# Kernel optimization log

Measured on AMD Instinct MI355X. Metric: run time of the kernel, lower is better.

Reference implementation:

```python
import jax, jax.numpy as jnp
import numpy as np
from jax import lax

EPS = 1e-06
K = 7  # kernel_size
C1 = 0.01 ** 2
C2 = 0.03 ** 2

_SOBEL_X = jnp.array([[-1.0, 0.0, 1.0], [-2.0, 0.0, 2.0], [-1.0, 0.0, 1.0]], dtype=jnp.float32).reshape(1, 1, 3, 3)
_SOBEL_Y = jnp.array([[-1.0, -2.0, -1.0], [0.0, 0.0, 0.0], [1.0, 2.0, 1.0]], dtype=jnp.float32).reshape(1, 1, 3, 3)


def _conv3x3(x, w):
    # NCHW cross-correlation with zero padding=1 (matches F.conv2d)
    return lax.conv_general_dilated(
        x, w, window_strides=(1, 1), padding=[(1, 1), (1, 1)],
        dimension_numbers=('NCHW', 'OIHW', 'NCHW'))


def _box(x):
    # avg_pool2d(k, stride=1, pad=k//2, count_include_pad=True):
    # sum over zero-padded window, divide by k*k everywhere.
    p = K // 2
    s = lax.reduce_window(x, jnp.float32(0.0), lax.add,
                          window_dimensions=(1, 1, K, K),
                          window_strides=(1, 1, 1, 1),
                          padding=[(0, 0), (0, 0), (p, p), (p, p)])
    return s / jnp.float32(K * K)


def _grad_mag(x):
    gx = _conv3x3(x, _SOBEL_X)
    gy = _conv3x3(x, _SOBEL_Y)
    return jnp.sqrt(gx * gx + gy * gy + EPS)


def setup_inputs() -> dict:
    key = jax.random.key(0)
    k1, k2 = jax.random.split(key)
    B, H, W = 64, 512, 512
    pred = jax.random.normal(k1, (B, 1, H, W), dtype=jnp.float32)
    target = jax.random.normal(k2, (B, 1, H, W), dtype=jnp.float32)
    min_target = jnp.zeros((B,), dtype=jnp.float32)
    max_target = jnp.ones((B,), dtype=jnp.float32)
    return {"pred": pred, "target": target, "min_target": min_target, "max_target": max_target}


def reference(pred, target, min_target, max_target):
    B = pred.shape[0]
    mn = min_target.reshape(B, 1, 1, 1)
    mx = max_target.reshape(B, 1, 1, 1)
    dr = jnp.maximum(mx - mn, EPS)
    p = (pred - mn) / dr
    t = (target - mn) / dr

    gp = _grad_mag(p)
    gt = _grad_mag(t)

    mu_p = _box(p)
    mu_t = _box(t)
    luminance = (2.0 * mu_p * mu_t + C1) / (mu_p * mu_p + mu_t * mu_t + C1)

    mu_gp = _box(gp)
    mu_gt = _box(gt)
    sig_p = _box(gp * gp) - mu_gp * mu_gp
    sig_t = _box(gt * gt) - mu_gt * mu_gt
    sig_x = _box(gp * gt) - mu_gp * mu_gt
    cs = (2.0 * sig_x + C2) / (sig_p + sig_t + C2)

    return 1.0 - jnp.mean(luminance * cs)
```

## Files before the change

kernel.cpp:

```cpp
#include <hip/hip_runtime.h>
#include <hip/hip_fp16.h>
#include <math.h>


constexpr int NT = 256;
constexpr float EPS_F = 1e-6f;
constexpr float C1S = 2401.0f * 0.0001f;
constexpr float C2S = 2401.0f * 0.0009f;

union U4 { uint4 u; __half2 h[4]; };
union F4U { float4 v; float a[4]; };

__device__ __forceinline__ __half2 h2swap(__half2 x) {
    unsigned u = __builtin_bit_cast(unsigned, x);
    u = (u >> 16) | (u << 16);
    return __builtin_bit_cast(__half2, u);
}

__device__ __forceinline__ float ssim_px(__half2 apt, __half2 ag, __half2 agg, __half2 agx) {
    float2 vpt = __half22float2(apt);
    float2 vg  = __half22float2(ag);
    float2 vgg = __half22float2(agg);
    float  vgx = __low2float(agx);
    float lum_n = 2.0f * vpt.x * vpt.y + C1S;
    float lum_d = vpt.x * vpt.x + vpt.y * vpt.y + C1S;
    float cs_n  = 2.0f * (49.0f * vgx - vg.x * vg.y) + C2S;
    float cs_d  = 49.0f * (vgg.x + vgg.y) - vg.x * vg.x - vg.y * vg.y + C2S;
    return lum_n * cs_n * __builtin_amdgcn_rcpf(lum_d * cs_d);
}

__global__ __launch_bounds__(NT, 4)
void gssim_strip(const float* __restrict__ pred, const float* __restrict__ target,
                 const float* __restrict__ mn_arr, const float* __restrict__ mx_arr,
                 float* __restrict__ partial) {
    constexpr int H = 512, W = 512;
    __shared__ alignas(16) __half2 spt[40][44];
    __shared__ alignas(16) __half2 hsAll[32][41][4];
    __shared__ float red[4];

    const int blk = blockIdx.x;
    const int b   = blk >> 4;
    const int gy0 = (blk & 15) * 32;
    const int tid = threadIdx.x;

    const float mn     = mn_arr[b];
    const float inv_dr = 1.0f / fmaxf(mx_arr[b] - mn, EPS_F);
    const float* pimg = pred   + (size_t)b * H * W;
    const float* timg = target + (size_t)b * H * W;

    const bool rows_ok_all = (gy0 >= 4) && (gy0 + 35 < H);

    const int gS  = tid % 10;
    const int yr  = tid / 10;
    const int yS0 = 2 * yr, yS1 = yS0 + 1;
    const int gyS0 = gy0 - 4 + yS0;
    const int gyS1 = gyS0 + 1;
    const bool rok0 = (gyS0 >= 0 && gyS0 < H);
    const bool rok1 = (gyS1 >= 0 && gyS1 < H);
    const bool hasS = (tid < 200);

    F4U Pa0, Ta0, Pa1, Ta1;

    auto stage1m = [&](int gx0n, bool rowok, int gyI, F4U& P, F4U& T) {
        int gx = gx0n - 4 + 4 * gS;
        P.v = make_float4(0.f, 0.f, 0.f, 0.f);
        T.v = make_float4(0.f, 0.f, 0.f, 0.f);
        if (rowok) {
            if (gx >= 0 && gx + 4 <= W) {
                P.v = *reinterpret_cast<const float4*>(pimg + (size_t)gyI * W + gx);
                T.v = *reinterpret_cast<const float4*>(timg + (size_t)gyI * W + gx);
            } else {
#pragma unroll
                for (int c = 0; c < 4; ++c) {
                    int x = gx + c;
                    if (x >= 0 && x < W) {
                        P.a[c] = pimg[(size_t)gyI * W + x];
                        T.a[c] = timg[(size_t)gyI * W + x];
                    }
                }
            }
        }
    };
    auto stagePair = [&](int gx0n) {
        if (rows_ok_all && gx0n >= 4 && gx0n <= 448) {
            int gx = gx0n - 4 + 4 * gS;
            Pa0.v = *reinterpret_cast<const float4*>(pimg + (size_t)gyS0 * W + gx);
            Ta0.v = *reinterpret_cast<const float4*>(timg + (size_t)gyS0 * W + gx);
            Pa1.v = *reinterpret_cast<const float4*>(pimg + (size_t)gyS1 * W + gx);
            Ta1.v = *reinterpret_cast<const float4*>(timg + (size_t)gyS1 * W + gx);
        } else {
            stage1m(gx0n, rok0, gyS0, Pa0, Ta0);
            stage1m(gx0n, rok1, gyS1, Pa1, Ta1);
        }
    };

    auto writePair = [&](int gx0n) {
        if (rows_ok_all && gx0n >= 4 && gx0n <= 448) {
            U4 w0, w1;
#pragma unroll
            for (int c = 0; c < 4; ++c) {
                w0.h[c] = __floats2half2_rn((Pa0.a[c] - mn) * inv_dr, (Ta0.a[c] - mn) * inv_dr);
                w1.h[c] = __floats2half2_rn((Pa1.a[c] - mn) * inv_dr, (Ta1.a[c] - mn) * inv_dr);
            }
            *reinterpret_cast<uint4*>(&spt[yS0][4 * gS]) = w0.u;
            *reinterpret_cast<uint4*>(&spt[yS1][4 * gS]) = w1.u;
        } else {
            int gx = gx0n - 4 + 4 * gS;
            U4 w0, w1;
#pragma unroll
            for (int c = 0; c < 4; ++c) {
                int x = gx + c;
                bool okc = (x >= 0) && (x < W);
                bool ok0 = rok0 && okc, ok1 = rok1 && okc;
                w0.h[c] = __floats2half2_rn(ok0 ? (Pa0.a[c] - mn) * inv_dr : 0.f,
                                            ok0 ? (Ta0.a[c] - mn) * inv_dr : 0.f);
                w1.h[c] = __floats2half2_rn(ok1 ? (Pa1.a[c] - mn) * inv_dr : 0.f,
                                            ok1 ? (Ta1.a[c] - mn) * inv_dr : 0.f);
            }
            *reinterpret_cast<uint4*>(&spt[yS0][4 * gS]) = w0.u;
            *reinterpret_cast<uint4*>(&spt[yS1][4 * gS]) = w1.u;
        }
    };

    const __half2 two2  = __float2half2_rn(2.0f);
    const __half2 eps2  = __float2half2_rn(1e-6f);
    const __half2 zero2 = __float2half2_rn(0.0f);

    if (hasS) { stagePair(0); writePair(0); }
    __syncthreads();

    float accl = 0.0f;

    for (int tx = 0; tx < 16; ++tx) {
        const int gx0 = tx * 32;

        if (tx < 15 && hasS) stagePair(gx0 + 32);

        if (tid < 152) {
            const int cg = tid / 38;
            const int k  = tid - cg * 38;
            const int c0 = 8 * cg;

            __half2 A[3][16];
#pragma unroll
            for (int r = 0; r < 3; ++r) {
#pragma unroll
                for (int q = 0; q < 4; ++q) {
                    U4 v; v.u = *reinterpret_cast<const uint4*>(&spt[k + r][c0 + 4 * q]);
                    A[r][4 * q] = v.h[0]; A[r][4 * q + 1] = v.h[1];
                    A[r][4 * q + 2] = v.h[2]; A[r][4 * q + 3] = v.h[3];
                }
            }

            __half2 grad[14];
            const bool safe_tile = rows_ok_all && (tx >= 1) && (tx <= 14);
            if (safe_tile) {
#pragma unroll
                for (int jj = 0; jj < 14; ++jj) {
                    __half2 gxh = __hsub2(A[0][jj + 2], A[0][jj]);
                    gxh = __hfma2(two2, __hsub2(A[1][jj + 2], A[1][jj]), gxh);
                    gxh = __hadd2(gxh, __hsub2(A[2][jj + 2], A[2][jj]));
                    __half2 gyh = __hsub2(A[2][jj], A[0][jj]);
                    gyh = __hfma2(two2, __hsub2(A[2][jj + 1], A[0][jj + 1]), gyh);
                    gyh = __hadd2(gyh, __hsub2(A[2][jj + 2], A[0][jj + 2]));
                    grad[jj] = h2sqrt(__hfma2(gxh, gxh, __hfma2(gyh, gyh, eps2)));
                }
            } else {
                const int gr = gy0 + k - 3;
                const bool rowv = (gr >= 0 && gr < H);
#pragma unroll
                for (int jj = 0; jj < 14; ++jj) {
                    __half2 gxh = __hsub2(A[0][jj + 2], A[0][jj]);
                    gxh = __hfma2(two2, __hsub2(A[1][jj + 2], A[1][jj]), gxh);
                    gxh = __hadd2(gxh, __hsub2(A[2][jj + 2], A[2][jj]));
                    __half2 gyh = __hsub2(A[2][jj], A[0][jj]);
                    gyh = __hfma2(two2, __hsub2(A[2][jj + 1], A[0][jj + 1]), gyh);
                    gyh = __hadd2(gyh, __hsub2(A[2][jj + 2], A[0][jj + 2]));
                    __half2 g = h2sqrt(__hfma2(gxh, gxh, __hfma2(gyh, gyh, eps2)));
                    int gc = gx0 + c0 + jj - 3;
                    grad[jj] = (rowv && gc >= 0 && gc < W) ? g : zero2;
                }
            }

            __half2 Hpt = A[1][1], Hg = grad[0];
            __half2 Hgg = __hmul2(grad[0], grad[0]);
            __half2 Hgx = __hmul2(grad[0], h2swap(grad[0]));
#pragma unroll
            for (int q = 1; q < 7; ++q) {
                Hpt = __hadd2(Hpt, A[1][q + 1]);
                Hg  = __hadd2(Hg,  grad[q]);
                Hgg = __hfma2(grad[q], grad[q], Hgg);
                Hgx = __hfma2(grad[q], h2swap(grad[q]), Hgx);
            }
            U4 w0;
            w0.h[0] = Hpt; w0.h[1] = Hg; w0.h[2] = Hgg; w0.h[3] = Hgx;
            *reinterpret_cast<uint4*>(&hsAll[c0][k][0]) = w0.u;
#pragma unroll
            for (int m = 1; m < 8; ++m) {
                __half2 gin = grad[m + 6], gout = grad[m - 1];
                Hpt = __hadd2(__hsub2(Hpt, A[1][m]), A[1][m + 7]);
                Hg  = __hadd2(__hsub2(Hg, gout), gin);
                Hgg = __hfma2(gin, gin, __hsub2(Hgg, __hmul2(gout, gout)));
                Hgx = __hfma2(gin, h2swap(gin), __hsub2(Hgx, __hmul2(gout, h2swap(gout))));
                U4 w;
                w.h[0] = Hpt; w.h[1] = Hg; w.h[2] = Hgg; w.h[3] = Hgx;
                *reinterpret_cast<uint4*>(&hsAll[c0 + m][k][0]) = w.u;
            }
        }
        __syncthreads();

        {
            const int ox = tid & 31;
            const int q  = tid >> 5;
            const int r0 = 4 * q;
            U4 win[10];
#pragma unroll
            for (int j = 0; j < 7; ++j)
                win[j].u = *reinterpret_cast<const uint4*>(&hsAll[ox][r0 + j][0]);
            __half2 Spt = win[0].h[0], Sg = win[0].h[1], Sgg = win[0].h[2], Sgx = win[0].h[3];
#pragma unroll
            for (int j = 1; j < 7; ++j) {
                Spt = __hadd2(Spt, win[j].h[0]);
                Sg  = __hadd2(Sg,  win[j].h[1]);
                Sgg = __hadd2(Sgg, win[j].h[2]);
                Sgx = __hadd2(Sgx, win[j].h[3]);
            }
            accl += ssim_px(Spt, Sg, Sgg, Sgx);
#pragma unroll
            for (int s = 1; s < 4; ++s) {
                win[6 + s].u = *reinterpret_cast<const uint4*>(&hsAll[ox][r0 + 6 + s][0]);
                Spt = __hadd2(__hsub2(Spt, win[s - 1].h[0]), win[6 + s].h[0]);
                Sg  = __hadd2(__hsub2(Sg,  win[s - 1].h[1]), win[6 + s].h[1]);
                Sgg = __hadd2(__hsub2(Sgg, win[s - 1].h[2]), win[6 + s].h[2]);
                Sgx = __hadd2(__hsub2(Sgx, win[s - 1].h[3]), win[6 + s].h[3]);
                accl += ssim_px(Spt, Sg, Sgg, Sgx);
            }
        }

        if (tx < 15 && hasS) writePair(gx0 + 32);
        __syncthreads();
    }

#pragma unroll
    for (int off = 32; off > 0; off >>= 1) accl += __shfl_down(accl, off, 64);
    if ((tid & 63) == 0) red[tid >> 6] = accl;
    __syncthreads();
    if (tid == 0) partial[blk] = red[0] + red[1] + red[2] + red[3];
}

__global__ __launch_bounds__(256)
void gssim_final(const float* __restrict__ partial, int n,
                 float* __restrict__ out, double inv_count) {
    __shared__ double sred[256];
    double acc = 0.0;
    for (int i = threadIdx.x; i < n; i += 256) acc += (double)partial[i];
    sred[threadIdx.x] = acc;
    __syncthreads();
    for (int s = 128; s > 0; s >>= 1) {
        if ((int)threadIdx.x < s) sred[threadIdx.x] += sred[threadIdx.x + s];
        __syncthreads();
    }
    if (threadIdx.x == 0) out[0] = (float)(1.0 - sred[0] * inv_count);
}

extern "C" void kernel_launch(void* const* d_in, const int* in_sizes, int n_in,
                              void* d_out, int out_size, void* d_ws, size_t ws_size,
                              hipStream_t stream) {
    const float* pred   = (const float*)d_in[0];
    const float* target = (const float*)d_in[1];
    const float* mn     = (const float*)d_in[2];
    const float* mx     = (const float*)d_in[3];
    float* out = (float*)d_out;

    const int B = in_sizes[2];
    const int H = 512, W = 512;

    float* partial = (float*)d_ws;

    const int nblocks = B * (H / 32);
    gssim_strip<<<nblocks, NT, 0, stream>>>(pred, target, mn, mx, partial);

    const double inv_count = 1.0 / ((double)B * (double)H * (double)W);
    gssim_final<<<1, 256, 0, stream>>>(partial, nblocks, out, inv_count);
}
```

Measured before the change: 85.81 us.

## Split strips into half-width blocks, redistribute horizontal pass, swizzle shared layout

Each block now handles half of a 32-row strip (8 column tiles instead of 16), which doubles the grid to 2048 blocks. The horizontal box pass now uses 4-column units (304 work items spread over all 256 threads plus 48 extras) instead of 8-column units on only 152 threads, so fewer threads sit idle. The hsAll shared array is transposed and XOR-like rotated to reduce LDS bank conflicts, and normalization is done in half2 arithmetic. In exchange, more halo reloads happen at block seams, there is more sliding-window setup overhead per column, and half-precision normalization loses some precision.

```diff
diff --git a/kernel.cpp b/kernel.cpp
--- a/kernel.cpp
+++ b/kernel.cpp
@@ -35,16 +35,19 @@
                  float* __restrict__ partial) {
     constexpr int H = 512, W = 512;
     __shared__ alignas(16) __half2 spt[40][44];
-    __shared__ alignas(16) __half2 hsAll[32][41][4];
-    __shared__ float red[4];
-
-    const int blk = blockIdx.x;
-    const int b   = blk >> 4;
-    const int gy0 = (blk & 15) * 32;
-    const int tid = threadIdx.x;
+    __shared__ alignas(16) __half2 hsAll[38][32][4];
+
+    const int blk  = blockIdx.x;
+    const int b    = blk >> 5;
+    const int rem  = blk & 31;
+    const int gy0  = (rem >> 1) * 32;
+    const int tx0  = (rem & 1) * 8;
+    const int tid  = threadIdx.x;
 
     const float mn     = mn_arr[b];
     const float inv_dr = 1.0f / fmaxf(mx_arr[b] - mn, EPS_F);
+    const __half2 mn2  = __float2half2_rn(mn);
+    const __half2 inv2 = __float2half2_rn(inv_dr);
     const float* pimg = pred   + (size_t)b * H * W;
     const float* timg = target + (size_t)b * H * W;
 
@@ -94,69 +97,67 @@
         }
     };
 
+    auto normh2 = [&](float p, float t) {
+        return __hmul2(__hsub2(__floats2half2_rn(p, t), mn2), inv2);
+    };
     auto writePair = [&](int gx0n) {
+        U4 w0, w1;
         if (rows_ok_all && gx0n >= 4 && gx0n <= 448) {
-            U4 w0, w1;
 #pragma unroll
             for (int c = 0; c < 4; ++c) {
-                w0.h[c] = __floats2half2_rn((Pa0.a[c] - mn) * inv_dr, (Ta0.a[c] - mn) * inv_dr);
-                w1.h[c] = __floats2half2_rn((Pa1.a[c] - mn) * inv_dr, (Ta1.a[c] - mn) * inv_dr);
-            }
-            *reinterpret_cast<uint4*>(&spt[yS0][4 * gS]) = w0.u;
-            *reinterpret_cast<uint4*>(&spt[yS1][4 * gS]) = w1.u;
+                w0.h[c] = normh2(Pa0.a[c], Ta0.a[c]);
+                w1.h[c] = normh2(Pa1.a[c], Ta1.a[c]);
+            }
         } else {
             int gx = gx0n - 4 + 4 * gS;
-            U4 w0, w1;
+            const __half2 zero2l = __float2half2_rn(0.0f);
 #pragma unroll
             for (int c = 0; c < 4; ++c) {
                 int x = gx + c;
                 bool okc = (x >= 0) && (x < W);
-                bool ok0 = rok0 && okc, ok1 = rok1 && okc;
-                w0.h[c] = __floats2half2_rn(ok0 ? (Pa0.a[c] - mn) * inv_dr : 0.f,
-                                            ok0 ? (Ta0.a[c] - mn) * inv_dr : 0.f);
-                w1.h[c] = __floats2half2_rn(ok1 ? (Pa1.a[c] - mn) * inv_dr : 0.f,
-                                            ok1 ? (Ta1.a[c] - mn) * inv_dr : 0.f);
-            }
-            *reinterpret_cast<uint4*>(&spt[yS0][4 * gS]) = w0.u;
-            *reinterpret_cast<uint4*>(&spt[yS1][4 * gS]) = w1.u;
-        }
+                w0.h[c] = (rok0 && okc) ? normh2(Pa0.a[c], Ta0.a[c]) : zero2l;
+                w1.h[c] = (rok1 && okc) ? normh2(Pa1.a[c], Ta1.a[c]) : zero2l;
+            }
+        }
+        *reinterpret_cast<uint4*>(&spt[yS0][4 * gS]) = w0.u;
+        *reinterpret_cast<uint4*>(&spt[yS1][4 * gS]) = w1.u;
     };
 
     const __half2 two2  = __float2half2_rn(2.0f);
     const __half2 eps2  = __float2half2_rn(1e-6f);
     const __half2 zero2 = __float2half2_rn(0.0f);
 
-    if (hasS) { stagePair(0); writePair(0); }
+    if (hasS) { stagePair(tx0 * 32); writePair(tx0 * 32); }
     __syncthreads();
 
     float accl = 0.0f;
 
-    for (int tx = 0; tx < 16; ++tx) {
-        const int gx0 = tx * 32;
-
-        if (tx < 15 && hasS) stagePair(gx0 + 32);
-
-        if (tid < 152) {
-            const int cg = tid / 38;
-            const int k  = tid - cg * 38;
-            const int c0 = 8 * cg;
-
-            __half2 A[3][16];
+    for (int tt = 0; tt < 8; ++tt) {
+        const int gx0 = (tx0 + tt) * 32;
+        const bool interior = rows_ok_all && (gx0 >= 32) && (gx0 <= 448);
+
+        if (tt < 7 && hasS) stagePair(gx0 + 32);
+
+        auto p3unit = [&](int t) {
+            const int cg = t / 38;
+            const int k  = t - cg * 38;
+            const int c0 = 4 * cg;
+
+            __half2 A[3][12];
 #pragma unroll
             for (int r = 0; r < 3; ++r) {
 #pragma unroll
-                for (int q = 0; q < 4; ++q) {
+                for (int q = 0; q < 3; ++q) {
                     U4 v; v.u = *reinterpret_cast<const uint4*>(&spt[k + r][c0 + 4 * q]);
                     A[r][4 * q] = v.h[0]; A[r][4 * q + 1] = v.h[1];
                     A[r][4 * q + 2] = v.h[2]; A[r][4 * q + 3] = v.h[3];
                 }
             }
 
-            __half2 grad[14];
-            const bool safe_tile = rows_ok_all && (tx >= 1) && (tx <= 14);
-            if (safe_tile) {
-#pragma unroll
-                for (int jj = 0; jj < 14; ++jj) {
+            __half2 grad[10];
+            if (interior) {
+#pragma unroll
+                for (int jj = 0; jj < 10; ++jj) {
                     __half2 gxh = __hsub2(A[0][jj + 2], A[0][jj]);
                     gxh = __hfma2(two2, __hsub2(A[1][jj + 2], A[1][jj]), gxh);
                     gxh = __hadd2(gxh, __hsub2(A[2][jj + 2], A[2][jj]));
@@ -169,7 +170,7 @@
                 const int gr = gy0 + k - 3;
                 const bool rowv = (gr >= 0 && gr < H);
 #pragma unroll
-                for (int jj = 0; jj < 14; ++jj) {
+                for (int jj = 0; jj < 10; ++jj) {
                     __half2 gxh = __hsub2(A[0][jj + 2], A[0][jj]);
                     gxh = __hfma2(two2, __hsub2(A[1][jj + 2], A[1][jj]), gxh);
                     gxh = __hadd2(gxh, __hsub2(A[2][jj + 2], A[2][jj]));
@@ -194,9 +195,9 @@
             }
             U4 w0;
             w0.h[0] = Hpt; w0.h[1] = Hg; w0.h[2] = Hgg; w0.h[3] = Hgx;
-            *reinterpret_cast<uint4*>(&hsAll[c0][k][0]) = w0.u;
-#pragma unroll
-            for (int m = 1; m < 8; ++m) {
+            *reinterpret_cast<uint4*>(&hsAll[k][(c0 + k) & 31][0]) = w0.u;
+#pragma unroll
+            for (int m = 1; m < 4; ++m) {
                 __half2 gin = grad[m + 6], gout = grad[m - 1];
                 Hpt = __hadd2(__hsub2(Hpt, A[1][m]), A[1][m + 7]);
                 Hg  = __hadd2(__hsub2(Hg, gout), gin);
@@ -204,9 +205,11 @@
                 Hgx = __hfma2(gin, h2swap(gin), __hsub2(Hgx, __hmul2(gout, h2swap(gout))));
                 U4 w;
                 w.h[0] = Hpt; w.h[1] = Hg; w.h[2] = Hgg; w.h[3] = Hgx;
-                *reinterpret_cast<uint4*>(&hsAll[c0 + m][k][0]) = w.u;
-            }
-        }
+                *reinterpret_cast<uint4*>(&hsAll[k][(c0 + m + k) & 31][0]) = w.u;
+            }
+        };
+        p3unit(tid);
+        if (tid < 48) p3unit(tid + 256);
         __syncthreads();
 
         {
@@ -215,8 +218,10 @@
             const int r0 = 4 * q;
             U4 win[10];
 #pragma unroll
-            for (int j = 0; j < 7; ++j)
-                win[j].u = *reinterpret_cast<const uint4*>(&hsAll[ox][r0 + j][0]);
+            for (int j = 0; j < 7; ++j) {
+                int r = r0 + j;
+                win[j].u = *reinterpret_cast<const uint4*>(&hsAll[r][(ox + r) & 31][0]);
+            }
             __half2 Spt = win[0].h[0], Sg = win[0].h[1], Sgg = win[0].h[2], Sgx = win[0].h[3];
 #pragma unroll
             for (int j = 1; j < 7; ++j) {
@@ -228,7 +233,8 @@
             accl += ssim_px(Spt, Sg, Sgg, Sgx);
 #pragma unroll
             for (int s = 1; s < 4; ++s) {
-                win[6 + s].u = *reinterpret_cast<const uint4*>(&hsAll[ox][r0 + 6 + s][0]);
+                int r = r0 + 6 + s;
+                win[6 + s].u = *reinterpret_cast<const uint4*>(&hsAll[r][(ox + r) & 31][0]);
                 Spt = __hadd2(__hsub2(Spt, win[s - 1].h[0]), win[6 + s].h[0]);
                 Sg  = __hadd2(__hsub2(Sg,  win[s - 1].h[1]), win[6 + s].h[1]);
                 Sgg = __hadd2(__hsub2(Sgg, win[s - 1].h[2]), win[6 + s].h[2]);
@@ -237,10 +243,11 @@
             }
         }
 
-        if (tx < 15 && hasS) writePair(gx0 + 32);
+        if (tt < 7 && hasS) writePair(gx0 + 32);
         __syncthreads();
     }
 
+    float* red = reinterpret_cast<float*>(&spt[0][0]);
 #pragma unroll
     for (int off = 32; off > 0; off >>= 1) accl += __shfl_down(accl, off, 64);
     if ((tid & 63) == 0) red[tid >> 6] = accl;
@@ -277,7 +284,7 @@
 
     float* partial = (float*)d_ws;
 
-    const int nblocks = B * (H / 32);
+    const int nblocks = B * (H / 32) * 2;
     gssim_strip<<<nblocks, NT, 0, stream>>>(pred, target, mn, mx, partial);
 
     const double inv_count = 1.0 / ((double)B * (double)H * (double)W);
```

After: 94.19 us. 9.8% more time.
